# Optimization experiments

Hardware: AMD Instinct MI355X
Metric: run time of the kernel (lower is better)

## Reference

```python
import jax, jax.numpy as jnp
import numpy as np

N = 50000       # nodes
E = 600000      # edges (before self-loops)
D_IN, D_H, D_OUT, D_E = 128, 128, 64, 8
NEG_SLOPE = 0.2


def _glorot(key, shape):
    fan = shape[0]
    return jax.random.normal(key, shape, dtype=jnp.float32) / jnp.sqrt(jnp.float32(fan))


def setup_inputs() -> dict:
    key = jax.random.key(0)
    ks = iter(jax.random.split(key, 32))
    inp = {
        "x": jax.random.normal(next(ks), (N, D_IN), dtype=jnp.float32),
        "edge_index": jax.random.randint(next(ks), (2, E), 0, N, dtype=jnp.int64),
        "edge_attr": jax.random.normal(next(ks), (E, D_E), dtype=jnp.float32),
    }
    dims = [(D_IN, D_H), (D_H, D_H), (D_H, D_OUT)]  # 3 GATConv layers, heads=1
    for i, (din, dout) in enumerate(dims):
        inp[f"W{i}"] = _glorot(next(ks), (din, dout))
        inp[f"as{i}"] = _glorot(next(ks), (dout,))
        inp[f"ad{i}"] = _glorot(next(ks), (dout,))
        inp[f"We{i}"] = _glorot(next(ks), (D_E, dout))
        inp[f"ae{i}"] = _glorot(next(ks), (dout,))
        inp[f"b{i}"] = jnp.zeros((dout,), dtype=jnp.float32)
    return inp


def _add_self_loops(src, dst, edge_attr, n):
    # PyG add_self_loops(fill_value='mean'): self-loop attr = mean of incoming edge attrs
    deg = jax.ops.segment_sum(jnp.ones_like(dst, dtype=edge_attr.dtype), dst, num_segments=n)
    mean_attr = jax.ops.segment_sum(edge_attr, dst, num_segments=n) / jnp.maximum(deg, 1.0)[:, None]
    loop = jnp.arange(n, dtype=src.dtype)
    return (jnp.concatenate([src, loop]),
            jnp.concatenate([dst, loop]),
            jnp.concatenate([edge_attr, mean_attr], axis=0))


def _gat_layer(x, src, dst, edge_attr, W, a_s, a_d, We, a_e, b, n):
    h = x @ W                                   # [N, C] linear projection
    alpha = (h @ a_s)[src] + (h @ a_d)[dst] + (edge_attr @ We) @ a_e   # [Etot]
    alpha = jax.nn.leaky_relu(alpha, NEG_SLOPE)
    m = jax.ops.segment_max(alpha, dst, num_segments=n)                # segment softmax over dst
    ex = jnp.exp(alpha - m[dst])
    denom = jax.ops.segment_sum(ex, dst, num_segments=n)
    w = ex / (denom[dst] + 1e-16)
    return jax.ops.segment_sum(h[src] * w[:, None], dst, num_segments=n) + b


def reference(x, edge_index, edge_attr,
              W0, as0, ad0, We0, ae0, b0,
              W1, as1, ad1, We1, ae1, b1,
              W2, as2, ad2, We2, ae2, b2):
    n = x.shape[0]
    src, dst, ea = _add_self_loops(edge_index[0], edge_index[1], edge_attr, n)
    h = jax.nn.relu(_gat_layer(x, src, dst, ea, W0, as0, ad0, We0, ae0, b0, n))
    h = jax.nn.relu(_gat_layer(h, src, dst, ea, W1, as1, ad1, We1, ae1, b1, n))
    return _gat_layer(h, src, dst, ea, W2, as2, ad2, We2, ae2, b2, n)
```

## Files before the change

### kernel.cpp

```cpp
#include <hip/hip_runtime.h>
#include <hip/hip_fp16.h>
#include <cstdint>

#define NEG_SLOPE 0.2f
#define LOG2E 1.4426950408889634f
#define MAXD 64

typedef _Float16 f16;
typedef __attribute__((ext_vector_type(8))) _Float16 f16x8;
typedef __attribute__((ext_vector_type(4))) float f32x4;


__global__ void k_count(const int* __restrict__ dst, int* __restrict__ deg,
                        unsigned short* __restrict__ rank, int E) {
    int e = blockIdx.x * blockDim.x + threadIdx.x;
    if (e < E) {
        int r = atomicAdd(deg + dst[e], 1);
        rank[e] = (unsigned short)(r > MAXD - 1 ? MAXD - 1 : r);
    }
}

__global__ void k_wt(const float* __restrict__ W0, const float* __restrict__ W1,
                     const float* __restrict__ W2, f16* __restrict__ Wt0,
                     f16* __restrict__ Wt1, f16* __restrict__ Wt2,
                     const float* __restrict__ We0, const float* __restrict__ ae0,
                     const float* __restrict__ We1, const float* __restrict__ ae1,
                     const float* __restrict__ We2, const float* __restrict__ ae2,
                     float* __restrict__ wea, int* __restrict__ deg, int n) {
    int i = blockIdx.x * 256 + threadIdx.x;
    if (i < 16384) {
        int k = i >> 7, c = i & 127;
        Wt0[c * 128 + k] = (f16)W0[i];
    } else if (i < 32768) {
        int j = i - 16384; int k = j >> 7, c = j & 127;
        Wt1[c * 128 + k] = (f16)W1[j];
    } else if (i < 40960) {
        int j = i - 32768; int k = j >> 6, c = j & 63;
        Wt2[c * 128 + k] = (f16)W2[j];
    } else if (i < 40984) {
        int j = i - 40960;
        int layer = j >> 3, k = j & 7;
        const float* We = layer == 0 ? We0 : (layer == 1 ? We1 : We2);
        const float* ae = layer == 0 ? ae0 : (layer == 1 ? ae1 : ae2);
        int D = layer == 2 ? 64 : 128;
        float s = 0.f;
        for (int t = 0; t < D; t++) s = fmaf(We[(size_t)k * D + t], ae[t], s);
        wea[j] = s;
    } else if (i >= 41216) {
        int j = i - 41216;
        if (j < n) deg[j] = 0;
    }
}


__device__ __forceinline__ void fill_body(
    int bid, int tid,
    const int* __restrict__ src, const int* __restrict__ dst,
    const unsigned short* __restrict__ rank, const float* __restrict__ ea,
    const float* __restrict__ wea, ushort4* __restrict__ ed, int E)
{
    int e = bid * 256 + tid;
    if (e >= E) return;
    int s = src[e];
    int pos = dst[e] * MAXD + (int)rank[e];
    float4 a0 = *(const float4*)&ea[(size_t)e * 8];
    float4 a1 = *(const float4*)&ea[(size_t)e * 8 + 4];
    float4 w00 = *(const float4*)&wea[0],  w01 = *(const float4*)&wea[4];
    float4 w10 = *(const float4*)&wea[8],  w11 = *(const float4*)&wea[12];
    float4 w20 = *(const float4*)&wea[16], w21 = *(const float4*)&wea[20];
    float d0 = a0.x*w00.x + a0.y*w00.y + a0.z*w00.z + a0.w*w00.w
             + a1.x*w01.x + a1.y*w01.y + a1.z*w01.z + a1.w*w01.w;
    float d1 = a0.x*w10.x + a0.y*w10.y + a0.z*w10.z + a0.w*w10.w
             + a1.x*w11.x + a1.y*w11.y + a1.z*w11.z + a1.w*w11.w;
    float d2 = a0.x*w20.x + a0.y*w20.y + a0.z*w20.z + a0.w*w20.w
             + a1.x*w21.x + a1.y*w21.y + a1.z*w21.z + a1.w*w21.w;
    ushort4 rec;
    rec.x = (unsigned short)s;
    rec.y = __half_as_ushort(__float2half(d0));
    rec.z = __half_as_ushort(__float2half(d1));
    rec.w = __half_as_ushort(__float2half(d2));
    ed[pos] = rec;
}

template<int DOUT, bool XHALF>
__device__ __forceinline__ void gemm_mfma_body(
    int bid, int tid,
    const void* __restrict__ X_, const f16* __restrict__ Wt,
    const float* __restrict__ as_, const float* __restrict__ ad_,
    __half* __restrict__ H, float* __restrict__ hs, float* __restrict__ hd, int n)
{
    constexpr int NT = DOUT / 16;
    int lane = tid & 63;
    int wave = tid >> 6;
    int row0 = (bid * 4 + wave) * 16;
    if (row0 >= n) return;
    int lrow = lane & 15;
    int kgrp = lane >> 4;
    int arow = row0 + lrow;
    bool aok = arow < n;

    f32x4 acc[NT] = {};

#pragma unroll
    for (int kt = 0; kt < 128; kt += 32) {
        f16x8 a = {};
        if (aok) {
            if constexpr (XHALF) {
                a = *(const f16x8*)((const f16*)X_ + (size_t)arow * 128 + kt + 8 * kgrp);
            } else {
                const float* xp = (const float*)X_ + (size_t)arow * 128 + kt + 8 * kgrp;
                float4 x0 = *(const float4*)xp;
                float4 x1 = *(const float4*)(xp + 4);
                f16x8 t = { (f16)x0.x, (f16)x0.y, (f16)x0.z, (f16)x0.w,
                            (f16)x1.x, (f16)x1.y, (f16)x1.z, (f16)x1.w };
                a = t;
            }
        }
#pragma unroll
        for (int nt = 0; nt < NT; nt++) {
            f16x8 b = *(const f16x8*)(Wt + (size_t)(nt * 16 + lrow) * 128 + kt + 8 * kgrp);
            acc[nt] = __builtin_amdgcn_mfma_f32_16x16x32_f16(a, b, acc[nt], 0, 0, 0);
        }
    }

    float asv[NT], adv[NT];
#pragma unroll
    for (int nt = 0; nt < NT; nt++) {
        asv[nt] = as_[nt * 16 + lrow];
        adv[nt] = ad_[nt * 16 + lrow];
    }

#pragma unroll
    for (int r = 0; r < 4; r++) {
        int row = row0 + 4 * kgrp + r;
        bool rok = row < n;
        float ps = 0.f, pd = 0.f;
#pragma unroll
        for (int nt = 0; nt < NT; nt++) {
            float v = acc[nt][r];
            ps = fmaf(v, asv[nt], ps);
            pd = fmaf(v, adv[nt], pd);
            if (rok) H[(size_t)row * DOUT + nt * 16 + lrow] = __float2half(v);
        }
#pragma unroll
        for (int off = 8; off; off >>= 1) {
            ps += __shfl_xor(ps, off);
            pd += __shfl_xor(pd, off);
        }
        if (rok && lrow == 0) { hs[row] = ps; hd[row] = pd; }
    }
}

template<int DOUT, bool XHALF>
__global__ __launch_bounds__(256) void k_gemm_mfma(
    const void* __restrict__ X_, const f16* __restrict__ Wt,
    const float* __restrict__ as_, const float* __restrict__ ad_,
    __half* __restrict__ H, float* __restrict__ hs, float* __restrict__ hd, int n)
{
    gemm_mfma_body<DOUT, XHALF>(blockIdx.x, threadIdx.x, X_, Wt, as_, ad_, H, hs, hd, n);
}

__global__ __launch_bounds__(256) void k_fill_gemm0(
    const int* __restrict__ src, const int* __restrict__ dst,
    const unsigned short* __restrict__ rank, const float* __restrict__ ea,
    const float* __restrict__ wea, ushort4* __restrict__ ed, int E,
    const float* __restrict__ X, const f16* __restrict__ Wt0,
    const float* __restrict__ as_, const float* __restrict__ ad_,
    __half* __restrict__ H, float* __restrict__ hs, float* __restrict__ hd, int n,
    int gemmBlocks, int totalBlocks)
{
    int bid = blockIdx.x, tid = threadIdx.x;
    long long g = gemmBlocks, T = totalBlocks;
    int before = (int)((long long)bid * g / T);
    int after  = (int)(((long long)bid + 1) * g / T);
    if (after > before) {
        gemm_mfma_body<128, false>(before, tid, X, Wt0, as_, ad_, H, hs, hd, n);
    } else {
        fill_body(bid - before, tid, src, dst, rank, ea, wea, ed, E);
    }
}


template<int CPL>
__device__ __forceinline__ void accum_row16(float* acc, const __half* __restrict__ hrow,
                                            int l, float w) {
    if constexpr (CPL == 8) {
        float4 raw = *(const float4*)(hrow + 8 * l);
        __half2* h = (__half2*)&raw;
#pragma unroll
        for (int i = 0; i < 4; i++) {
            float2 f = __half22float2(h[i]);
            acc[2 * i]     = fmaf(w, f.x, acc[2 * i]);
            acc[2 * i + 1] = fmaf(w, f.y, acc[2 * i + 1]);
        }
    } else {
        float2 raw = *(const float2*)(hrow + 4 * l);
        __half2* h = (__half2*)&raw;
#pragma unroll
        for (int i = 0; i < 2; i++) {
            float2 f = __half22float2(h[i]);
            acc[2 * i]     = fmaf(w, f.x, acc[2 * i]);
            acc[2 * i + 1] = fmaf(w, f.y, acc[2 * i + 1]);
        }
    }
}

__device__ __forceinline__ float unpack_w(unsigned int p) {
    return __half2float(__ushort_as_half((unsigned short)(p & 0xFFFFu)));
}

__device__ __forceinline__ float fexp(float x) {
    return exp2f(x * LOG2E);
}

__device__ __forceinline__ float leaky(float a) {
    return a > 0.f ? a : NEG_SLOPE * a;
}

template<int DOUT, bool RELU, int LCOMP, bool OUT_HALF>
__global__ void k_aggregate(const __half* __restrict__ H,
                            const int* __restrict__ deg, const ushort4* __restrict__ edata,
                            const float* __restrict__ hs, const float* __restrict__ hd,
                            const float* __restrict__ bias, void* __restrict__ out_, int n) {
    int t = blockIdx.x * blockDim.x + threadIdx.x;
    int w = t >> 6, lane = t & 63;
    if (2 * w >= n) return;
    int half = lane >> 5, ln = lane & 31;
    int node = 2 * w + half;
    bool active = node < n;
    int d = active ? deg[node] : 0; if (d > MAXD) d = MAXD;
    int start = node << 6;
    float hdv = active ? hd[node] : 0.f;
    float hsw = active ? hs[node] : 0.f;
    int q = ln >> 4, l = ln & 15;

    constexpr int CPL = DOUT / 16;
    float acc[CPL] = {};
    float denom;

    int dmx = d;
    dmx = max(dmx, __shfl_xor(dmx, 32));

    if (dmx <= 32) {
        float al = -3.0e38f; int s = 0; float eadv = 0.f;
        if (ln < d) {
            ushort4 pv = edata[start + ln];
            s = pv.x;
            unsigned short eu = (LCOMP == 1) ? pv.y : (LCOMP == 2) ? pv.z : pv.w;
            eadv = __half2float(__ushort_as_half(eu));
            al = leaky(hs[s] + hdv + eadv);
        }
        float esum = (ln < d) ? eadv : 0.f;
        float m0 = al;
#pragma unroll
        for (int off = 16; off; off >>= 1) {
            esum += __shfl_xor(esum, off);
            m0 = fmaxf(m0, __shfl_xor(m0, off));
        }
        int dd = d < 1 ? 1 : d;
        float aself = leaky(hsw + hdv + esum / (float)dd);
        float m = fmaxf(m0, aself);

        float ex = (ln < d) ? fexp(al - m) : 0.f;
        float exsum = ex;
#pragma unroll
        for (int off = 16; off; off >>= 1) exsum += __shfl_xor(exsum, off);
        float exself = fexp(aself - m);
        denom = exsum + exself;

        unsigned int pk = ((unsigned int)s << 16) |
                          (unsigned int)__half_as_ushort(__float2half(ex));

        if (active && q == 0) accum_row16<CPL>(acc, H + (size_t)node * DOUT, l, exself);

        int pairs = (d + 1) >> 1;
#pragma unroll 4
        for (int jj = 0; jj < pairs; jj++) {
            int j = 2 * jj + q;
            unsigned int pj = (unsigned int)__shfl((int)pk, half * 32 + j);
            int sj = pj >> 16;
            float wt = unpack_w(pj);
            if (j < d) accum_row16<CPL>(acc, H + (size_t)sj * DOUT, l, wt);
        }
    } else {
        float esum = 0.f, m0 = -3.0e38f;
        for (int base = 0; base < d; base += 32) {
            if (base + ln < d) {
                ushort4 pv = edata[start + base + ln];
                unsigned short eu = (LCOMP == 1) ? pv.y : (LCOMP == 2) ? pv.z : pv.w;
                float ev = __half2float(__ushort_as_half(eu));
                esum += ev;
                m0 = fmaxf(m0, leaky(hs[pv.x] + hdv + ev));
            }
        }
#pragma unroll
        for (int off = 16; off; off >>= 1) {
            esum += __shfl_xor(esum, off);
            m0 = fmaxf(m0, __shfl_xor(m0, off));
        }
        int dd = d < 1 ? 1 : d;
        float aself = leaky(hsw + hdv + esum / (float)dd);
        float m = fmaxf(m0, aself);
        float exself = fexp(aself - m);
        denom = exself;
        if (active && q == 0) accum_row16<CPL>(acc, H + (size_t)node * DOUT, l, exself);

        int dw = dmx;
        for (int base = 0; base < dw; base += 32) {
            float ex = 0.f; int s = 0;
            if (base + ln < d) {
                ushort4 pv = edata[start + base + ln];
                s = pv.x;
                unsigned short eu = (LCOMP == 1) ? pv.y : (LCOMP == 2) ? pv.z : pv.w;
                ex = fexp(leaky(hs[s] + hdv + __half2float(__ushort_as_half(eu))) - m);
            }
            float exsum = ex;
#pragma unroll
            for (int off = 16; off; off >>= 1) exsum += __shfl_xor(exsum, off);
            denom += exsum;
            unsigned int pk = ((unsigned int)s << 16) |
                              (unsigned int)__half_as_ushort(__float2half(ex));
            int rem = d - base; if (rem > 32) rem = 32; if (rem < 0) rem = 0;
            int pairs = (rem + 1) >> 1;
            int pmax = pairs; pmax = max(pmax, __shfl_xor(pmax, 32));
#pragma unroll 4
            for (int jj = 0; jj < pmax; jj++) {
                int j = 2 * jj + q;
                unsigned int pj = (unsigned int)__shfl((int)pk, half * 32 + j);
                int sj = pj >> 16;
                float wt = unpack_w(pj);
                if (j < rem) accum_row16<CPL>(acc, H + (size_t)sj * DOUT, l, wt);
            }
        }
    }

#pragma unroll
    for (int v = 0; v < CPL; v++) acc[v] += __shfl_xor(acc[v], 16);

    if (active && q == 0) {
        float inv = 1.0f / (denom + 1e-16f);
        float o[CPL];
#pragma unroll
        for (int v = 0; v < CPL; v++) {
            o[v] = acc[v] * inv + bias[CPL * l + v];
            if (RELU) o[v] = fmaxf(o[v], 0.f);
        }
        if constexpr (OUT_HALF) {
            __half* outh = (__half*)out_;
            __half2 p[CPL / 2];
#pragma unroll
            for (int v = 0; v < CPL / 2; v++) p[v] = __floats2half2_rn(o[2 * v], o[2 * v + 1]);
            if constexpr (CPL == 8) {
                *(uint4*)&outh[(size_t)node * DOUT + 8 * l] = *(uint4*)p;
            } else {
                *(uint2*)&outh[(size_t)node * DOUT + 4 * l] = *(uint2*)p;
            }
        } else {
            float* outf = (float*)out_;
            if constexpr (CPL == 8) {
                float4 o0 = { o[0], o[1], o[2], o[3] };
                float4 o1 = { o[4], o[5], o[6], o[7] };
                *(float4*)&outf[(size_t)node * DOUT + 8 * l] = o0;
                *(float4*)&outf[(size_t)node * DOUT + 8 * l + 4] = o1;
            } else {
                float4 ov = { o[0], o[1], o[2], o[3] };
                *(float4*)&outf[(size_t)node * DOUT + 4 * l] = ov;
            }
        }
    }
}


extern "C" void kernel_launch(void* const* d_in, const int* in_sizes, int n_in,
                              void* d_out, int out_size, void* d_ws, size_t ws_size,
                              hipStream_t stream) {
    const float* x     = (const float*)d_in[0];
    const int*   eidx  = (const int*)d_in[1];
    const float* eattr = (const float*)d_in[2];
    const int N = in_sizes[0] / 128;
    const int E = in_sizes[1] / 2;
    const int* src = eidx;
    const int* dst = eidx + E;

    char* ws = (char*)d_ws;
    size_t off = 0;
    auto alloc = [&](size_t bytes) -> void* {
        void* p = ws + off;
        off += (bytes + 255) & ~(size_t)255;
        return p;
    };
    __half*         bufA = (__half*)alloc((size_t)N * 128 * sizeof(__half));
    __half*         hbuf = (__half*)alloc((size_t)N * 128 * sizeof(__half));
    int*            deg  = (int*)alloc((size_t)N * sizeof(int));
    float*          hs   = (float*)alloc((size_t)N * sizeof(float));
    float*          hd   = (float*)alloc((size_t)N * sizeof(float));
    ushort4*        ed   = (ushort4*)alloc((size_t)N * MAXD * sizeof(ushort4));
    unsigned short* rank = (unsigned short*)alloc((size_t)E * sizeof(unsigned short));
    f16*            Wt0  = (f16*)alloc(16384 * sizeof(f16));
    f16*            Wt1  = (f16*)alloc(16384 * sizeof(f16));
    f16*            Wt2  = (f16*)alloc(8192 * sizeof(f16));
    float*          wea  = (float*)alloc(64 * sizeof(float));

    const int tb = 256;

    int wt_blocks = 161 + (N + 255) / 256;
    k_wt<<<wt_blocks, 256, 0, stream>>>((const float*)d_in[3], (const float*)d_in[9],
                                        (const float*)d_in[15], Wt0, Wt1, Wt2,
                                        (const float*)d_in[6], (const float*)d_in[7],
                                        (const float*)d_in[12], (const float*)d_in[13],
                                        (const float*)d_in[18], (const float*)d_in[19],
                                        wea, deg, N);
    k_count<<<(E + tb - 1) / tb, tb, 0, stream>>>(dst, deg, rank, E);

    int agg_blocks = (N + 7) / 8;
    int gemm_blocks = (N + 63) / 64;

    {
        const float* as_ = (const float*)d_in[4];
        const float* ad_ = (const float*)d_in[5];
        int fillBlocks = (E + tb - 1) / tb;
        int totalBlocks = fillBlocks + gemm_blocks;
        k_fill_gemm0<<<totalBlocks, tb, 0, stream>>>(
            src, dst, rank, eattr, wea, ed, E,
            x, Wt0, as_, ad_, hbuf, hs, hd, N,
            gemm_blocks, totalBlocks);
        const float* b = (const float*)d_in[8];
        k_aggregate<128, true, 1, true><<<agg_blocks, tb, 0, stream>>>(hbuf, deg, ed, hs, hd, b, bufA, N);
    }
    {
        const float* as_ = (const float*)d_in[10];
        const float* ad_ = (const float*)d_in[11];
        const float* b   = (const float*)d_in[14];
        k_gemm_mfma<128, true><<<gemm_blocks, 256, 0, stream>>>(bufA, Wt1, as_, ad_, hbuf, hs, hd, N);
        k_aggregate<128, true, 2, true><<<agg_blocks, tb, 0, stream>>>(hbuf, deg, ed, hs, hd, b, bufA, N);
    }
    {
        const float* as_ = (const float*)d_in[16];
        const float* ad_ = (const float*)d_in[17];
        const float* b   = (const float*)d_in[20];
        k_gemm_mfma<64, true><<<gemm_blocks, 256, 0, stream>>>(bufA, Wt2, as_, ad_, hbuf, hs, hd, N);
        k_aggregate<64, false, 3, false><<<agg_blocks, tb, 0, stream>>>(hbuf, deg, ed, hs, hd, b, d_out, N);
    }
}
```

Baseline: 213.2 us.

## Fuse all stages into one cooperative persistent megakernel with grid syncs

Replaces the chain of eight kernel launches with a single cooperative kernel whose grid-stride loops over virtual blocks run every stage, separated by grid.sync(). The goal is to remove per-launch overhead and the drain/fill gaps between dependent kernels. In exchange, occupancy is capped by the cooperative grid size and launch_bounds(256,4), and the GEMM and aggregate bodies now share one register allocation. The old multi-kernel path is kept as a fallback if the cooperative launch fails.

```diff
diff --git a/kernel.cpp b/kernel.cpp
--- a/kernel.cpp
+++ b/kernel.cpp
@@ -1,6 +1,9 @@
 #include <hip/hip_runtime.h>
+#include <hip/hip_cooperative_groups.h>
 #include <hip/hip_fp16.h>
 #include <cstdint>
+
+namespace cg = cooperative_groups;
 
 #define NEG_SLOPE 0.2f
 #define LOG2E 1.4426950408889634f
@@ -11,23 +14,15 @@
 typedef __attribute__((ext_vector_type(4))) float f32x4;
 
 
-__global__ void k_count(const int* __restrict__ dst, int* __restrict__ deg,
-                        unsigned short* __restrict__ rank, int E) {
-    int e = blockIdx.x * blockDim.x + threadIdx.x;
-    if (e < E) {
-        int r = atomicAdd(deg + dst[e], 1);
-        rank[e] = (unsigned short)(r > MAXD - 1 ? MAXD - 1 : r);
-    }
-}
-
-__global__ void k_wt(const float* __restrict__ W0, const float* __restrict__ W1,
-                     const float* __restrict__ W2, f16* __restrict__ Wt0,
-                     f16* __restrict__ Wt1, f16* __restrict__ Wt2,
-                     const float* __restrict__ We0, const float* __restrict__ ae0,
-                     const float* __restrict__ We1, const float* __restrict__ ae1,
-                     const float* __restrict__ We2, const float* __restrict__ ae2,
-                     float* __restrict__ wea, int* __restrict__ deg, int n) {
-    int i = blockIdx.x * 256 + threadIdx.x;
+__device__ __forceinline__ void wt_item(
+    int i, const float* __restrict__ W0, const float* __restrict__ W1,
+    const float* __restrict__ W2, f16* __restrict__ Wt0, f16* __restrict__ Wt1,
+    f16* __restrict__ Wt2,
+    const float* __restrict__ We0, const float* __restrict__ ae0,
+    const float* __restrict__ We1, const float* __restrict__ ae1,
+    const float* __restrict__ We2, const float* __restrict__ ae2,
+    float* __restrict__ wea)
+{
     if (i < 16384) {
         int k = i >> 7, c = i & 127;
         Wt0[c * 128 + k] = (f16)W0[i];
@@ -46,12 +41,8 @@
         float s = 0.f;
         for (int t = 0; t < D; t++) s = fmaf(We[(size_t)k * D + t], ae[t], s);
         wea[j] = s;
-    } else if (i >= 41216) {
-        int j = i - 41216;
-        if (j < n) deg[j] = 0;
-    }
-}
-
+    }
+}
 
 __device__ __forceinline__ void fill_body(
     int bid, int tid,
@@ -151,13 +142,222 @@
     }
 }
 
-template<int DOUT, bool XHALF>
-__global__ __launch_bounds__(256) void k_gemm_mfma(
-    const void* __restrict__ X_, const f16* __restrict__ Wt,
-    const float* __restrict__ as_, const float* __restrict__ ad_,
-    __half* __restrict__ H, float* __restrict__ hs, float* __restrict__ hd, int n)
+
+template<int CPL>
+__device__ __forceinline__ void accum_row16(float* acc, const __half* __restrict__ hrow,
+                                            int l, float w) {
+    if constexpr (CPL == 8) {
+        float4 raw = *(const float4*)(hrow + 8 * l);
+        __half2* h = (__half2*)&raw;
+#pragma unroll
+        for (int i = 0; i < 4; i++) {
+            float2 f = __half22float2(h[i]);
+            acc[2 * i]     = fmaf(w, f.x, acc[2 * i]);
+            acc[2 * i + 1] = fmaf(w, f.y, acc[2 * i + 1]);
+        }
+    } else {
+        float2 raw = *(const float2*)(hrow + 4 * l);
+        __half2* h = (__half2*)&raw;
+#pragma unroll
+        for (int i = 0; i < 2; i++) {
+            float2 f = __half22float2(h[i]);
+            acc[2 * i]     = fmaf(w, f.x, acc[2 * i]);
+            acc[2 * i + 1] = fmaf(w, f.y, acc[2 * i + 1]);
+        }
+    }
+}
+
+__device__ __forceinline__ float unpack_w(unsigned int p) {
+    return __half2float(__ushort_as_half((unsigned short)(p & 0xFFFFu)));
+}
+
+__device__ __forceinline__ float fexp(float x) {
+    return exp2f(x * LOG2E);
+}
+
+__device__ __forceinline__ float leaky(float a) {
+    return a > 0.f ? a : NEG_SLOPE * a;
+}
+
+template<int DOUT, bool RELU, int LCOMP, bool OUT_HALF>
+__device__ __forceinline__ void agg_body(
+    int bid, int tid,
+    const __half* __restrict__ H, const int* __restrict__ deg,
+    const ushort4* __restrict__ edata, const float* __restrict__ hs,
+    const float* __restrict__ hd, const float* __restrict__ bias,
+    void* __restrict__ out_, int n)
 {
-    gemm_mfma_body<DOUT, XHALF>(blockIdx.x, threadIdx.x, X_, Wt, as_, ad_, H, hs, hd, n);
+    int w = bid * 4 + (tid >> 6), lane = tid & 63;
+    if (2 * w >= n) return;
+    int half = lane >> 5, ln = lane & 31;
+    int node = 2 * w + half;
+    bool active = node < n;
+    int d = active ? deg[node] : 0; if (d > MAXD) d = MAXD;
+    int start = node << 6;
+    float hdv = active ? hd[node] : 0.f;
+    float hsw = active ? hs[node] : 0.f;
+    int q = ln >> 4, l = ln & 15;
+
+    constexpr int CPL = DOUT / 16;
+    float acc[CPL] = {};
+    float denom;
+
+    int dmx = d;
+    dmx = max(dmx, __shfl_xor(dmx, 32));
+
+    if (dmx <= 32) {
+        float al = -3.0e38f; int s = 0; float eadv = 0.f;
+        if (ln < d) {
+            ushort4 pv = edata[start + ln];
+            s = pv.x;
+            unsigned short eu = (LCOMP == 1) ? pv.y : (LCOMP == 2) ? pv.z : pv.w;
+            eadv = __half2float(__ushort_as_half(eu));
+            al = leaky(hs[s] + hdv + eadv);
+        }
+        float esum = (ln < d) ? eadv : 0.f;
+        float m0 = al;
+#pragma unroll
+        for (int off = 16; off; off >>= 1) {
+            esum += __shfl_xor(esum, off);
+            m0 = fmaxf(m0, __shfl_xor(m0, off));
+        }
+        int dd = d < 1 ? 1 : d;
+        float aself = leaky(hsw + hdv + esum / (float)dd);
+        float m = fmaxf(m0, aself);
+
+        float ex = (ln < d) ? fexp(al - m) : 0.f;
+        float exsum = ex;
+#pragma unroll
+        for (int off = 16; off; off >>= 1) exsum += __shfl_xor(exsum, off);
+        float exself = fexp(aself - m);
+        denom = exsum + exself;
+
+        unsigned int pk = ((unsigned int)s << 16) |
+                          (unsigned int)__half_as_ushort(__float2half(ex));
+
+        if (active && q == 0) accum_row16<CPL>(acc, H + (size_t)node * DOUT, l, exself);
+
+        int pairs = (d + 1) >> 1;
+#pragma unroll 4
+        for (int jj = 0; jj < pairs; jj++) {
+            int j = 2 * jj + q;
+            unsigned int pj = (unsigned int)__shfl((int)pk, half * 32 + j);
+            int sj = pj >> 16;
+            float wt = unpack_w(pj);
+            if (j < d) accum_row16<CPL>(acc, H + (size_t)sj * DOUT, l, wt);
+        }
+    } else {
+        float esum = 0.f, m0 = -3.0e38f;
+        for (int base = 0; base < d; base += 32) {
+            if (base + ln < d) {
+                ushort4 pv = edata[start + base + ln];
+                unsigned short eu = (LCOMP == 1) ? pv.y : (LCOMP == 2) ? pv.z : pv.w;
+                float ev = __half2float(__ushort_as_half(eu));
+                esum += ev;
+                m0 = fmaxf(m0, leaky(hs[pv.x] + hdv + ev));
+            }
+        }
+#pragma unroll
+        for (int off = 16; off; off >>= 1) {
+            esum += __shfl_xor(esum, off);
+            m0 = fmaxf(m0, __shfl_xor(m0, off));
+        }
+        int dd = d < 1 ? 1 : d;
+        float aself = leaky(hsw + hdv + esum / (float)dd);
+        float m = fmaxf(m0, aself);
+        float exself = fexp(aself - m);
+        denom = exself;
+        if (active && q == 0) accum_row16<CPL>(acc, H + (size_t)node * DOUT, l, exself);
+
+        int dw = dmx;
+        for (int base = 0; base < dw; base += 32) {
+            float ex = 0.f; int s = 0;
+            if (base + ln < d) {
+                ushort4 pv = edata[start + base + ln];
+                s = pv.x;
+                unsigned short eu = (LCOMP == 1) ? pv.y : (LCOMP == 2) ? pv.z : pv.w;
+                ex = fexp(leaky(hs[s] + hdv + __half2float(__ushort_as_half(eu))) - m);
+            }
+            float exsum = ex;
+#pragma unroll
+            for (int off = 16; off; off >>= 1) exsum += __shfl_xor(exsum, off);
+            denom += exsum;
+            unsigned int pk = ((unsigned int)s << 16) |
+                              (unsigned int)__half_as_ushort(__float2half(ex));
+            int rem = d - base; if (rem > 32) rem = 32; if (rem < 0) rem = 0;
+            int pairs = (rem + 1) >> 1;
+            int pmax = pairs; pmax = max(pmax, __shfl_xor(pmax, 32));
+#pragma unroll 4
+            for (int jj = 0; jj < pmax; jj++) {
+                int j = 2 * jj + q;
+                unsigned int pj = (unsigned int)__shfl((int)pk, half * 32 + j);
+                int sj = pj >> 16;
+                float wt = unpack_w(pj);
+                if (j < rem) accum_row16<CPL>(acc, H + (size_t)sj * DOUT, l, wt);
+            }
+        }
+    }
+
+#pragma unroll
+    for (int v = 0; v < CPL; v++) acc[v] += __shfl_xor(acc[v], 16);
+
+    if (active && q == 0) {
+        float inv = 1.0f / (denom + 1e-16f);
+        float o[CPL];
+#pragma unroll
+        for (int v = 0; v < CPL; v++) {
+            o[v] = acc[v] * inv + bias[CPL * l + v];
+            if (RELU) o[v] = fmaxf(o[v], 0.f);
+        }
+        if constexpr (OUT_HALF) {
+            __half* outh = (__half*)out_;
+            __half2 p[CPL / 2];
+#pragma unroll
+            for (int v = 0; v < CPL / 2; v++) p[v] = __floats2half2_rn(o[2 * v], o[2 * v + 1]);
+            if constexpr (CPL == 8) {
+                *(uint4*)&outh[(size_t)node * DOUT + 8 * l] = *(uint4*)p;
+            } else {
+                *(uint2*)&outh[(size_t)node * DOUT + 4 * l] = *(uint2*)p;
+            }
+        } else {
+            float* outf = (float*)out_;
+            if constexpr (CPL == 8) {
+                float4 o0 = { o[0], o[1], o[2], o[3] };
+                float4 o1 = { o[4], o[5], o[6], o[7] };
+                *(float4*)&outf[(size_t)node * DOUT + 8 * l] = o0;
+                *(float4*)&outf[(size_t)node * DOUT + 8 * l + 4] = o1;
+            } else {
+                float4 ov = { o[0], o[1], o[2], o[3] };
+                *(float4*)&outf[(size_t)node * DOUT + 4 * l] = ov;
+            }
+        }
+    }
+}
+
+
+__global__ void k_wt(const float* __restrict__ W0, const float* __restrict__ W1,
+                     const float* __restrict__ W2, f16* __restrict__ Wt0,
+                     f16* __restrict__ Wt1, f16* __restrict__ Wt2,
+                     const float* __restrict__ We0, const float* __restrict__ ae0,
+                     const float* __restrict__ We1, const float* __restrict__ ae1,
+                     const float* __restrict__ We2, const float* __restrict__ ae2,
+                     float* __restrict__ wea, int* __restrict__ deg, int n) {
+    int i = blockIdx.x * 256 + threadIdx.x;
+    if (i < 41216) {
+        wt_item(i, W0, W1, W2, Wt0, Wt1, Wt2, We0, ae0, We1, ae1, We2, ae2, wea);
+    } else {
+        int j = i - 41216;
+        if (j < n) deg[j] = 0;
+    }
+}
+
+__global__ void k_count(const int* __restrict__ dst, int* __restrict__ deg,
+                        unsigned short* __restrict__ rank, int E) {
+    int e = blockIdx.x * blockDim.x + threadIdx.x;
+    if (e < E) {
+        int r = atomicAdd(deg + dst[e], 1);
+        rank[e] = (unsigned short)(r > MAXD - 1 ? MAXD - 1 : r);
+    }
 }
 
 __global__ __launch_bounds__(256) void k_fill_gemm0(
@@ -180,41 +380,13 @@
     }
 }
 
-
-template<int CPL>
-__device__ __forceinline__ void accum_row16(float* acc, const __half* __restrict__ hrow,
-                                            int l, float w) {
-    if constexpr (CPL == 8) {
-        float4 raw = *(const float4*)(hrow + 8 * l);
-        __half2* h = (__half2*)&raw;
-#pragma unroll
-        for (int i = 0; i < 4; i++) {
-            float2 f = __half22float2(h[i]);
-            acc[2 * i]     = fmaf(w, f.x, acc[2 * i]);
-            acc[2 * i + 1] = fmaf(w, f.y, acc[2 * i + 1]);
-        }
-    } else {
-        float2 raw = *(const float2*)(hrow + 4 * l);
-        __half2* h = (__half2*)&raw;
-#pragma unroll
-        for (int i = 0; i < 2; i++) {
-            float2 f = __half22float2(h[i]);
-            acc[2 * i]     = fmaf(w, f.x, acc[2 * i]);
-            acc[2 * i + 1] = fmaf(w, f.y, acc[2 * i + 1]);
-        }
-    }
-}
-
-__device__ __forceinline__ float unpack_w(unsigned int p) {
-    return __half2float(__ushort_as_half((unsigned short)(p & 0xFFFFu)));
-}
-
-__device__ __forceinline__ float fexp(float x) {
-    return exp2f(x * LOG2E);
-}
-
-__device__ __forceinline__ float leaky(float a) {
-    return a > 0.f ? a : NEG_SLOPE * a;
+template<int DOUT, bool XHALF>
+__global__ __launch_bounds__(256) void k_gemm_mfma(
+    const void* __restrict__ X_, const f16* __restrict__ Wt,
+    const float* __restrict__ as_, const float* __restrict__ ad_,
+    __half* __restrict__ H, float* __restrict__ hs, float* __restrict__ hd, int n)
+{
+    gemm_mfma_body<DOUT, XHALF>(blockIdx.x, threadIdx.x, X_, Wt, as_, ad_, H, hs, hd, n);
 }
 
 template<int DOUT, bool RELU, int LCOMP, bool OUT_HALF>
@@ -222,152 +394,75 @@
                             const int* __restrict__ deg, const ushort4* __restrict__ edata,
                             const float* __restrict__ hs, const float* __restrict__ hd,
                             const float* __restrict__ bias, void* __restrict__ out_, int n) {
-    int t = blockIdx.x * blockDim.x + threadIdx.x;
-    int w = t >> 6, lane = t & 63;
-    if (2 * w >= n) return;
-    int half = lane >> 5, ln = lane & 31;
-    int node = 2 * w + half;
-    bool active = node < n;
-    int d = active ? deg[node] : 0; if (d > MAXD) d = MAXD;
-    int start = node << 6;
-    float hdv = active ? hd[node] : 0.f;
-    float hsw = active ? hs[node] : 0.f;
-    int q = ln >> 4, l = ln & 15;
-
-    constexpr int CPL = DOUT / 16;
-    float acc[CPL] = {};
-    float denom;
-
-    int dmx = d;
-    dmx = max(dmx, __shfl_xor(dmx, 32));
-
-    if (dmx <= 32) {
-        float al = -3.0e38f; int s = 0; float eadv = 0.f;
-        if (ln < d) {
-            ushort4 pv = edata[start + ln];
-            s = pv.x;
-            unsigned short eu = (LCOMP == 1) ? pv.y : (LCOMP == 2) ? pv.z : pv.w;
-            eadv = __half2float(__ushort_as_half(eu));
-            al = leaky(hs[s] + hdv + eadv);
-        }
-        float esum = (ln < d) ? eadv : 0.f;
-        float m0 = al;
-#pragma unroll
-        for (int off = 16; off; off >>= 1) {
-            esum += __shfl_xor(esum, off);
-            m0 = fmaxf(m0, __shfl_xor(m0, off));
-        }
-        int dd = d < 1 ? 1 : d;
-        float aself = leaky(hsw + hdv + esum / (float)dd);
-        float m = fmaxf(m0, aself);
-
-        float ex = (ln < d) ? fexp(al - m) : 0.f;
-        float exsum = ex;
-#pragma unroll
-        for (int off = 16; off; off >>= 1) exsum += __shfl_xor(exsum, off);
-        float exself = fexp(aself - m);
-        denom = exsum + exself;
-
-        unsigned int pk = ((unsigned int)s << 16) |
-                          (unsigned int)__half_as_ushort(__float2half(ex));
-
-        if (active && q == 0) accum_row16<CPL>(acc, H + (size_t)node * DOUT, l, exself);
-
-        int pairs = (d + 1) >> 1;
-#pragma unroll 4
-        for (int jj = 0; jj < pairs; jj++) {
-            int j = 2 * jj + q;
-            unsigned int pj = (unsigned int)__shfl((int)pk, half * 32 + j);
-            int sj = pj >> 16;
-            float wt = unpack_w(pj);
-            if (j < d) accum_row16<CPL>(acc, H + (size_t)sj * DOUT, l, wt);
-        }
-    } else {
-        float esum = 0.f, m0 = -3.0e38f;
-        for (int base = 0; base < d; base += 32) {
-            if (base + ln < d) {
-                ushort4 pv = edata[start + base + ln];
-                unsigned short eu = (LCOMP == 1) ? pv.y : (LCOMP == 2) ? pv.z : pv.w;
-                float ev = __half2float(__ushort_as_half(eu));
-                esum += ev;
-                m0 = fmaxf(m0, leaky(hs[pv.x] + hdv + ev));
-            }
-        }
-#pragma unroll
-        for (int off = 16; off; off >>= 1) {
-            esum += __shfl_xor(esum, off);
-            m0 = fmaxf(m0, __shfl_xor(m0, off));
-        }
-        int dd = d < 1 ? 1 : d;
-        float aself = leaky(hsw + hdv + esum / (float)dd);
-        float m = fmaxf(m0, aself);
-        float exself = fexp(aself - m);
-        denom = exself;
-        if (active && q == 0) accum_row16<CPL>(acc, H + (size_t)node * DOUT, l, exself);
-
-        int dw = dmx;
-        for (int base = 0; base < dw; base += 32) {
-            float ex = 0.f; int s = 0;
-            if (base + ln < d) {
-                ushort4 pv = edata[start + base + ln];
-                s = pv.x;
-                unsigned short eu = (LCOMP == 1) ? pv.y : (LCOMP == 2) ? pv.z : pv.w;
-                ex = fexp(leaky(hs[s] + hdv + __half2float(__ushort_as_half(eu))) - m);
-            }
-            float exsum = ex;
-#pragma unroll
-            for (int off = 16; off; off >>= 1) exsum += __shfl_xor(exsum, off);
-            denom += exsum;
-            unsigned int pk = ((unsigned int)s << 16) |
-                              (unsigned int)__half_as_ushort(__float2half(ex));
-            int rem = d - base; if (rem > 32) rem = 32; if (rem < 0) rem = 0;
-            int pairs = (rem + 1) >> 1;
-            int pmax = pairs; pmax = max(pmax, __shfl_xor(pmax, 32));
-#pragma unroll 4
-            for (int jj = 0; jj < pmax; jj++) {
-                int j = 2 * jj + q;
-                unsigned int pj = (unsigned int)__shfl((int)pk, half * 32 + j);
-                int sj = pj >> 16;
-                float wt = unpack_w(pj);
-                if (j < rem) accum_row16<CPL>(acc, H + (size_t)sj * DOUT, l, wt);
-            }
-        }
-    }
-
-#pragma unroll
-    for (int v = 0; v < CPL; v++) acc[v] += __shfl_xor(acc[v], 16);
-
-    if (active && q == 0) {
-        float inv = 1.0f / (denom + 1e-16f);
-        float o[CPL];
-#pragma unroll
-        for (int v = 0; v < CPL; v++) {
-            o[v] = acc[v] * inv + bias[CPL * l + v];
-            if (RELU) o[v] = fmaxf(o[v], 0.f);
-        }
-        if constexpr (OUT_HALF) {
-            __half* outh = (__half*)out_;
-            __half2 p[CPL / 2];
-#pragma unroll
-            for (int v = 0; v < CPL / 2; v++) p[v] = __floats2half2_rn(o[2 * v], o[2 * v + 1]);
-            if constexpr (CPL == 8) {
-                *(uint4*)&outh[(size_t)node * DOUT + 8 * l] = *(uint4*)p;
-            } else {
-                *(uint2*)&outh[(size_t)node * DOUT + 4 * l] = *(uint2*)p;
-            }
+    agg_body<DOUT, RELU, LCOMP, OUT_HALF>(blockIdx.x, threadIdx.x, H, deg, edata,
+                                          hs, hd, bias, out_, n);
+}
+
+
+struct Params {
+    const float* x; const int* src; const int* dst; const float* ea;
+    const float *W0, *as0, *ad0, *We0, *ae0, *b0;
+    const float *W1, *as1, *ad1, *We1, *ae1, *b1;
+    const float *W2, *as2, *ad2, *We2, *ae2, *b2;
+    float* out;
+    __half* bufA; __half* hbuf; int* deg; float* hs; float* hd;
+    ushort4* ed; unsigned short* rank;
+    f16 *Wt0, *Wt1, *Wt2; float* wea;
+    int N, E;
+    int vb_wt, vb_zero, vb_count, vb_fill, vb_gemm, vb_agg;
+};
+
+__global__ __launch_bounds__(256, 4) void k_mega(Params p) {
+    cg::grid_group grid = cg::this_grid();
+    int tid = threadIdx.x;
+
+    for (int vb = blockIdx.x; vb < p.vb_wt + p.vb_zero; vb += gridDim.x) {
+        if (vb < p.vb_wt) {
+            wt_item(vb * 256 + tid, p.W0, p.W1, p.W2, p.Wt0, p.Wt1, p.Wt2,
+                    p.We0, p.ae0, p.We1, p.ae1, p.We2, p.ae2, p.wea);
         } else {
-            float* outf = (float*)out_;
-            if constexpr (CPL == 8) {
-                float4 o0 = { o[0], o[1], o[2], o[3] };
-                float4 o1 = { o[4], o[5], o[6], o[7] };
-                *(float4*)&outf[(size_t)node * DOUT + 8 * l] = o0;
-                *(float4*)&outf[(size_t)node * DOUT + 8 * l + 4] = o1;
-            } else {
-                float4 ov = { o[0], o[1], o[2], o[3] };
-                *(float4*)&outf[(size_t)node * DOUT + 4 * l] = ov;
-            }
-        }
-    }
+            int j = (vb - p.vb_wt) * 256 + tid;
+            if (j < p.N) p.deg[j] = 0;
+        }
+    }
+    grid.sync();
+
+    for (int vb = blockIdx.x; vb < p.vb_count; vb += gridDim.x) {
+        int e = vb * 256 + tid;
+        if (e < p.E) {
+            int r = atomicAdd(p.deg + p.dst[e], 1);
+            p.rank[e] = (unsigned short)(r > MAXD - 1 ? MAXD - 1 : r);
+        }
+    }
+    grid.sync();
+
+    for (int vb = blockIdx.x; vb < p.vb_fill + p.vb_gemm; vb += gridDim.x) {
+        if (vb < p.vb_fill)
+            fill_body(vb, tid, p.src, p.dst, p.rank, p.ea, p.wea, p.ed, p.E);
+        else
+            gemm_mfma_body<128, false>(vb - p.vb_fill, tid, p.x, p.Wt0, p.as0, p.ad0,
+                                       p.hbuf, p.hs, p.hd, p.N);
+    }
+    grid.sync();
+
+    for (int vb = blockIdx.x; vb < p.vb_agg; vb += gridDim.x)
+        agg_body<128, true, 1, true>(vb, tid, p.hbuf, p.deg, p.ed, p.hs, p.hd, p.b0, p.bufA, p.N);
+    grid.sync();
+
+    for (int vb = blockIdx.x; vb < p.vb_gemm; vb += gridDim.x)
+        gemm_mfma_body<128, true>(vb, tid, p.bufA, p.Wt1, p.as1, p.ad1, p.hbuf, p.hs, p.hd, p.N);
+    grid.sync();
+
+    for (int vb = blockIdx.x; vb < p.vb_agg; vb += gridDim.x)
+        agg_body<128, true, 2, true>(vb, tid, p.hbuf, p.deg, p.ed, p.hs, p.hd, p.b1, p.bufA, p.N);
+    grid.sync();
+
+    for (int vb = blockIdx.x; vb < p.vb_gemm; vb += gridDim.x)
+        gemm_mfma_body<64, true>(vb, tid, p.bufA, p.Wt2, p.as2, p.ad2, p.hbuf, p.hs, p.hd, p.N);
+    grid.sync();
+
+    for (int vb = blockIdx.x; vb < p.vb_agg; vb += gridDim.x)
+        agg_body<64, false, 3, false>(vb, tid, p.hbuf, p.deg, p.ed, p.hs, p.hd, p.b2, p.out, p.N);
 }
 
 
@@ -402,43 +497,56 @@
     float*          wea  = (float*)alloc(64 * sizeof(float));
 
     const int tb = 256;
-
-    int wt_blocks = 161 + (N + 255) / 256;
-    k_wt<<<wt_blocks, 256, 0, stream>>>((const float*)d_in[3], (const float*)d_in[9],
-                                        (const float*)d_in[15], Wt0, Wt1, Wt2,
-                                        (const float*)d_in[6], (const float*)d_in[7],
-                                        (const float*)d_in[12], (const float*)d_in[13],
-                                        (const float*)d_in[18], (const float*)d_in[19],
-                                        wea, deg, N);
-    k_count<<<(E + tb - 1) / tb, tb, 0, stream>>>(dst, deg, rank, E);
-
-    int agg_blocks = (N + 7) / 8;
-    int gemm_blocks = (N + 63) / 64;
-
-    {
-        const float* as_ = (const float*)d_in[4];
-        const float* ad_ = (const float*)d_in[5];
+    int vb_wt = 161;
+    int vb_zero = (N + 255) / 256;
+    int vb_count = (E + 255) / 256;
+    int vb_fill = (E + 255) / 256;
+    int vb_gemm = (N + 63) / 64;
+    int vb_agg = (N + 7) / 8;
+
+    Params p;
+    p.x = x; p.src = src; p.dst = dst; p.ea = eattr;
+    p.W0 = (const float*)d_in[3];  p.as0 = (const float*)d_in[4];  p.ad0 = (const float*)d_in[5];
+    p.We0 = (const float*)d_in[6]; p.ae0 = (const float*)d_in[7];  p.b0 = (const float*)d_in[8];
+    p.W1 = (const float*)d_in[9];  p.as1 = (const float*)d_in[10]; p.ad1 = (const float*)d_in[11];
+    p.We1 = (const float*)d_in[12]; p.ae1 = (const float*)d_in[13]; p.b1 = (const float*)d_in[14];
+    p.W2 = (const float*)d_in[15]; p.as2 = (const float*)d_in[16]; p.ad2 = (const float*)d_in[17];
+    p.We2 = (const float*)d_in[18]; p.ae2 = (const float*)d_in[19]; p.b2 = (const float*)d_in[20];
+    p.out = (float*)d_out;
+    p.bufA = bufA; p.hbuf = hbuf; p.deg = deg; p.hs = hs; p.hd = hd;
+    p.ed = ed; p.rank = rank; p.Wt0 = Wt0; p.Wt1 = Wt1; p.Wt2 = Wt2; p.wea = wea;
+    p.N = N; p.E = E;
+    p.vb_wt = vb_wt; p.vb_zero = vb_zero; p.vb_count = vb_count;
+    p.vb_fill = vb_fill; p.vb_gemm = vb_gemm; p.vb_agg = vb_agg;
+
+    int maxB = 0;
+    hipError_t oerr = hipOccupancyMaxActiveBlocksPerMultiprocessor(&maxB, (const void*)k_mega, 256, 0);
+    bool coop_ok = false;
+    if (oerr == hipSuccess && maxB > 0) {
+        int grid = maxB * 256;
+        int want = vb_agg;
+        if (grid > want) grid = want;
+        void* args[] = { (void*)&p };
+        hipError_t lerr = hipLaunchCooperativeKernel((const void*)k_mega, dim3(grid), dim3(256),
+                                                     args, 0, stream);
+        coop_ok = (lerr == hipSuccess);
+    }
+
+    if (!coop_ok) {
+        int wt_blocks = 161 + (N + 255) / 256;
+        k_wt<<<wt_blocks, 256, 0, stream>>>(p.W0, p.W1, p.W2, Wt0, Wt1, Wt2,
+                                            p.We0, p.ae0, p.We1, p.ae1, p.We2, p.ae2,
+                                            wea, deg, N);
+        k_count<<<(E + tb - 1) / tb, tb, 0, stream>>>(dst, deg, rank, E);
         int fillBlocks = (E + tb - 1) / tb;
-        int totalBlocks = fillBlocks + gemm_blocks;
+        int totalBlocks = fillBlocks + vb_gemm;
         k_fill_gemm0<<<totalBlocks, tb, 0, stream>>>(
             src, dst, rank, eattr, wea, ed, E,
-            x, Wt0, as_, ad_, hbuf, hs, hd, N,
-            gemm_blocks, totalBlocks);
-        const float* b = (const float*)d_in[8];
-        k_aggregate<128, true, 1, true><<<agg_blocks, tb, 0, stream>>>(hbuf, deg, ed, hs, hd, b, bufA, N);
-    }
-    {
-        const float* as_ = (const float*)d_in[10];
-        const float* ad_ = (const float*)d_in[11];
-        const float* b   = (const float*)d_in[14];
-        k_gemm_mfma<128, true><<<gemm_blocks, 256, 0, stream>>>(bufA, Wt1, as_, ad_, hbuf, hs, hd, N);
-        k_aggregate<128, true, 2, true><<<agg_blocks, tb, 0, stream>>>(hbuf, deg, ed, hs, hd, b, bufA, N);
-    }
-    {
-        const float* as_ = (const float*)d_in[16];
-        const float* ad_ = (const float*)d_in[17];
-        const float* b   = (const float*)d_in[20];
-        k_gemm_mfma<64, true><<<gemm_blocks, 256, 0, stream>>>(bufA, Wt2, as_, ad_, hbuf, hs, hd, N);
-        k_aggregate<64, false, 3, false><<<agg_blocks, tb, 0, stream>>>(hbuf, deg, ed, hs, hd, b, d_out, N);
-    }
-}
+            x, Wt0, p.as0, p.ad0, hbuf, hs, hd, N, vb_gemm, totalBlocks);
+        k_aggregate<128, true, 1, true><<<vb_agg, tb, 0, stream>>>(hbuf, deg, ed, hs, hd, p.b0, bufA, N);
+        k_gemm_mfma<128, true><<<vb_gemm, 256, 0, stream>>>(bufA, Wt1, p.as1, p.ad1, hbuf, hs, hd, N);
+        k_aggregate<128, true, 2, true><<<vb_agg, tb, 0, stream>>>(hbuf, deg, ed, hs, hd, p.b1, bufA, N);
+        k_gemm_mfma<64, true><<<vb_gemm, 256, 0, stream>>>(bufA, Wt2, p.as2, p.ad2, hbuf, hs, hd, N);
+        k_aggregate<64, false, 3, false><<<vb_agg, tb, 0, stream>>>(hbuf, deg, ed, hs, hd, p.b2, d_out, N);
+    }
+}
```

Result: slower. 730.3 us (+242.6%).
